# Optimization experiments

Hardware: AMD Instinct MI355X
Metric: run time of the kernel (lower is better)

Reference implementation:

```python
import jax, jax.numpy as jnp
import numpy as np

B, T, C, HS = 8, 2048, 1024, 128

def setup_inputs() -> dict:
    key = jax.random.key(0)
    kx, kq, kk, kv = jax.random.split(key, 4)
    x = jax.random.normal(kx, (B, T, C), dtype=jnp.float32)
    # torch Linear(C, HS, bias=False): y = x @ W^T with W [HS, C].
    # We store the transposed form [C, HS] and right-multiply (same math).
    scale = 1.0 / np.sqrt(C)  # torch default init scale-ish; exact init irrelevant for correctness
    Wq = jax.random.normal(kq, (C, HS), dtype=jnp.float32) * scale
    Wk = jax.random.normal(kk, (C, HS), dtype=jnp.float32) * scale
    Wv = jax.random.normal(kv, (C, HS), dtype=jnp.float32) * scale
    return {"x": x, "Wq": Wq, "Wk": Wk, "Wv": Wv}

def reference(x, Wq, Wk, Wv):
    Bx, Tx, Cx = x.shape
    q = x @ Wq  # [B, T, HS]
    k = x @ Wk
    v = x @ Wv
    # NOTE: original scales by C**-0.5 where C = n_embd (not head_size)
    wei = jnp.einsum('btd,bsd->bts', q, k) * (Cx ** -0.5)  # [B, T, T]
    causal = jnp.tril(jnp.ones((Tx, Tx), dtype=bool))
    wei = jnp.where(causal, wei, -jnp.inf)
    wei = jax.nn.softmax(wei, axis=-1)
    # dropout rate 0.0 (eval semantics) -> identity
    return jnp.einsum('bts,bsd->btd', wei, v)  # [B, T, HS]
```

## Files before the change

### kernel.cpp

```cpp
#include <hip/hip_runtime.h>
#include <hip/hip_bf16.h>
#include <stdint.h>

typedef float f32x4 __attribute__((ext_vector_type(4)));
typedef float f32x4v __attribute__((ext_vector_type(4)));
typedef short short8 __attribute__((ext_vector_type(8)));
typedef unsigned short u16;
typedef unsigned short u16x8 __attribute__((ext_vector_type(8)));
typedef unsigned short u16x4 __attribute__((ext_vector_type(4)));

#define MFMA16x16x32 __builtin_amdgcn_mfma_f32_16x16x32_bf16

__device__ __forceinline__ u16 f2bf(float f) {
    unsigned int u = __builtin_bit_cast(unsigned int, f);
    u += 0x7fffu + ((u >> 16) & 1u);
    return (u16)(u >> 16);
}
__device__ __forceinline__ float bf2f(u16 v) {
    unsigned int u = ((unsigned int)v) << 16;
    return __builtin_bit_cast(float, u);
}

__device__ __forceinline__ void gload_lds16(const void* g, void* l) {
    __builtin_amdgcn_global_load_lds(
        (const __attribute__((address_space(1))) uint32_t*)g,
        (__attribute__((address_space(3))) uint32_t*)l, 16, 0, 0);
}

__device__ __forceinline__ int z_small128(int p) {
    int na = (p + 2) >> 1;
    int za = (8 * na + 16) / 17;
    za = za < 1 ? 1 : za;
    return za > 7 ? 7 : za;
}

__global__ void k_transpose_wf(const float* __restrict__ Wq, const float* __restrict__ Wk,
                               const float* __restrict__ Wv, u16* __restrict__ WTf) {
    int tid  = blockIdx.x * 256 + threadIdx.x;
    int f    = tid >> 6;
    int lane = tid & 63;
    int kt  = f / 48;
    int rem = f % 48;
    int ks  = rem / 24;
    int nc  = rem % 24;
    int col = nc * 16 + (lane & 15);
    int w   = col >> 7, n = col & 127;
    int k0  = kt * 64 + ks * 32 + (lane >> 4) * 8;
    const float* W = (w == 0) ? Wq : ((w == 1) ? Wk : Wv);
    u16x8 v;
#pragma unroll
    for (int j = 0; j < 8; ++j)
        v[j] = f2bf(W[(size_t)(k0 + j) * 128 + n]);
    *(u16x8*)(&WTf[(size_t)tid * 8]) = v;
}

__global__ __launch_bounds__(512) void k_qkv_gemm8(
    const float* __restrict__ x, const u16* __restrict__ WTf,
    u16* __restrict__ qb, u16* __restrict__ kb, u16* __restrict__ vT)
{
    __shared__ u16 abuf[2][64 * 64];
    __shared__ u16 bbuf[2][384 * 64];
    const int tid  = threadIdx.x;
    const int lane = tid & 63, wid = tid >> 6;
    const int wr = wid >> 2, wc = wid & 3;
    const int lrow = lane & 15, lk = lane >> 4;
    const int m0 = blockIdx.x * 64;

    const int arow = tid >> 3;
    const int aseg = tid & 7;
    const float* xsrc = x + (size_t)(m0 + arow) * 1024 + aseg * 8;

    f32x4 acc[2][6];
#pragma unroll
    for (int i = 0; i < 2; ++i)
#pragma unroll
        for (int j = 0; j < 6; ++j) acc[i][j] = (f32x4){0.f, 0.f, 0.f, 0.f};

#define LOADA(s0, s1, ktv)                                                     \
    s0 = *(const f32x4v*)(xsrc + (ktv) * 64);                                  \
    s1 = *(const f32x4v*)(xsrc + (ktv) * 64 + 4);

#define STOREA(buf, s0, s1)                                                    \
    {   u16x8 v;                                                               \
        v[0]=f2bf(s0[0]); v[1]=f2bf(s0[1]); v[2]=f2bf(s0[2]); v[3]=f2bf(s0[3]); \
        v[4]=f2bf(s1[0]); v[5]=f2bf(s1[1]); v[6]=f2bf(s1[2]); v[7]=f2bf(s1[3]); \
        *(u16x8*)(&buf[arow * 64 + ((aseg ^ (arow & 7)) << 3)]) = v; }

#define ISSUEB(buf, ktv)                                                       \
    {   const u16* bsrc = WTf + (size_t)(ktv) * 24576;                         \
        _Pragma("unroll") for (int i = 0; i < 6; ++i) {                        \
            int c = tid + i * 512;                                             \
            gload_lds16(bsrc + c * 8, &buf[c * 8]);                            \
        } }

#define COMPUTE(ab, bb)                                                        \
    _Pragma("unroll") for (int ks = 0; ks < 2; ++ks) {                         \
        short8 af[2];                                                          \
        _Pragma("unroll") for (int mf = 0; mf < 2; ++mf) {                     \
            int row = wr * 32 + mf * 16 + lrow;                                \
            int blk = (ks * 4 + lk) ^ (row & 7);                               \
            af[mf] = *(const short8*)(&ab[row * 64 + (blk << 3)]);             \
        }                                                                      \
        _Pragma("unroll") for (int nf = 0; nf < 6; ++nf) {                     \
            short8 bfr = *(const short8*)(&bb[(ks * 24 + wc * 6 + nf) * 512 + lane * 8]); \
            _Pragma("unroll") for (int mf = 0; mf < 2; ++mf)                   \
                acc[mf][nf] = MFMA16x16x32(af[mf], bfr, acc[mf][nf], 0, 0, 0); \
        } }

#define WAITBAR()                                                              \
    asm volatile("s_waitcnt vmcnt(2) lgkmcnt(0)\n\ts_barrier" ::: "memory");   \
    __builtin_amdgcn_sched_barrier(0);

    f32x4v a0A, a1A, a0B, a1B;
    LOADA(a0A, a1A, 0);
    LOADA(a0B, a1B, 1);
    STOREA(abuf[0], a0A, a1A);
    ISSUEB(bbuf[0], 0);
    LOADA(a0A, a1A, 2);
    WAITBAR();

    for (int kt = 0; kt < 16; kt += 2) {
        {
            const int ktn = (kt + 1 < 16) ? kt + 1 : 15;
            ISSUEB(bbuf[1], ktn);
            __builtin_amdgcn_sched_barrier(0);
            COMPUTE(abuf[0], bbuf[0]);
            STOREA(abuf[1], a0B, a1B);
            const int kp = (kt + 3 < 16) ? kt + 3 : 15;
            LOADA(a0B, a1B, kp);
            WAITBAR();
        }
        {
            const int ktn = (kt + 2 < 16) ? kt + 2 : 15;
            ISSUEB(bbuf[0], ktn);
            __builtin_amdgcn_sched_barrier(0);
            COMPUTE(abuf[1], bbuf[1]);
            STOREA(abuf[0], a0A, a1A);
            const int kp = (kt + 4 < 16) ? kt + 4 : 15;
            LOADA(a0A, a1A, kp);
            WAITBAR();
        }
    }
#undef LOADA
#undef STOREA
#undef ISSUEB
#undef COMPUTE
#undef WAITBAR

#pragma unroll
    for (int nf = 0; nf < 6; ++nf) {
        const int gc   = wc * 96 + nf * 16 + lrow;
        const int wsel = gc >> 7;
        const int col  = gc & 127;
#pragma unroll
        for (int mf = 0; mf < 2; ++mf) {
            const int row0 = m0 + wr * 32 + mf * 16 + lk * 4;
            if (wsel == 0) {
#pragma unroll
                for (int jj = 0; jj < 4; ++jj)
                    qb[(size_t)(row0 + jj) * 128 + col] = f2bf(acc[mf][nf][jj]);
            } else if (wsel == 1) {
#pragma unroll
                for (int jj = 0; jj < 4; ++jj)
                    kb[(size_t)(row0 + jj) * 128 + col] = f2bf(acc[mf][nf][jj]);
            } else {
                const int bb = row0 >> 11, t0 = row0 & 2047;
                u16x4 v;
#pragma unroll
                for (int jj = 0; jj < 4; ++jj) v[jj] = f2bf(acc[mf][nf][jj]);
                *(u16x4*)(&vT[((size_t)bb * 128 + col) * 2048 + t0]) = v;
            }
        }
    }
}

__global__ __launch_bounds__(256) void k_flash9(
    const u16* __restrict__ qb, const u16* __restrict__ kb, const u16* __restrict__ vT,
    u16* __restrict__ po, float* __restrict__ pm, float* __restrict__ pl)
{
    __shared__ u16 k_lds[128 * 128];
    __shared__ u16 v_lds[128 * 128];
    __shared__ u16 p_lds[4 * 16 * 128];
    const int tid  = threadIdx.x;
    const int lane = tid & 63, wid = tid >> 6;
    const int lrow = lane & 15, lk = lane >> 4;
    const int bx = blockIdx.x;
    const int b  = bx & 7;
    const int p  = (bx >> 3) & 15;
    const int z  = bx >> 7;

    const int za = z_small128(p);
    int qt, n, k, Z;
    if (z < za) { qt = p;      n = (p + 2) >> 1;  k = z;      Z = za;     }
    else        { qt = 31 - p; n = (33 - p) >> 1; k = z - za; Z = 8 - za; }
    const int t0 = (k * n) / Z;
    const int t1 = ((k + 1) * n) / Z;

    const int qrow0 = qt * 64;
    short8 qf[4];
    {
        const u16* qp = qb + ((size_t)b * 2048 + qrow0 + wid * 16 + lrow) * 128;
#pragma unroll
        for (int ks = 0; ks < 4; ++ks) qf[ks] = *(const short8*)(qp + ks * 32 + lk * 8);
    }
    f32x4 of[8];
#pragma unroll
    for (int i = 0; i < 8; ++i) of[i] = (f32x4){0.f, 0.f, 0.f, 0.f};
    float mrun[4], lsum[4];
#pragma unroll
    for (int j = 0; j < 4; ++j) { mrun[j] = -1e30f; lsum[j] = 0.f; }

    const u16* kbase = kb + (size_t)b * 2048 * 128;
    const u16* vbase = vT + (size_t)b * 128 * 2048;
    u16* pw = p_lds + wid * (16 * 128);

    for (int t = t0; t < t1; ++t) {
        const int kv0 = t << 7;
        __syncthreads();
#pragma unroll
        for (int i = 0; i < 8; ++i) {
            int ch = tid + i * 256;
            int row = ch >> 4, blk = ch & 15;
            gload_lds16(kbase + (size_t)(kv0 + row) * 128 + ((blk ^ (row & 7)) << 3),
                        &k_lds[ch * 8]);
        }
#pragma unroll
        for (int i = 0; i < 8; ++i) {
            int ch = tid + i * 256;
            int row = ch >> 4, blk = ch & 15;
            gload_lds16(vbase + (size_t)row * 2048 + kv0 + ((blk ^ (row & 7)) << 3),
                        &v_lds[ch * 8]);
        }
        __syncthreads();

        f32x4 sf[8];
#pragma unroll
        for (int nf = 0; nf < 8; ++nf) sf[nf] = (f32x4){0.f, 0.f, 0.f, 0.f};
#pragma unroll
        for (int ks = 0; ks < 4; ++ks)
#pragma unroll
            for (int nf = 0; nf < 8; ++nf) {
                int row = nf * 16 + lrow;
                int blk = (ks * 4 + lk) ^ (row & 7);
                short8 bfr = *(const short8*)(&k_lds[row * 128 + (blk << 3)]);
                sf[nf] = MFMA16x16x32(qf[ks], bfr, sf[nf], 0, 0, 0);
            }

        const bool needmask = (kv0 + 127 > qrow0 + wid * 16);
#pragma unroll
        for (int nf = 0; nf < 8; ++nf)
#pragma unroll
            for (int jj = 0; jj < 4; ++jj) {
                float s = sf[nf][jj] * 0.03125f;
                if (needmask &&
                    (kv0 + nf * 16 + lrow > qrow0 + wid * 16 + lk * 4 + jj)) s = -1e30f;
                sf[nf][jj] = s;
            }
        float mt[4];
#pragma unroll
        for (int jj = 0; jj < 4; ++jj) {
            float m01 = fmaxf(sf[0][jj], sf[1][jj]);
            float m23 = fmaxf(sf[2][jj], sf[3][jj]);
            float m45 = fmaxf(sf[4][jj], sf[5][jj]);
            float m67 = fmaxf(sf[6][jj], sf[7][jj]);
            mt[jj] = fmaxf(fmaxf(m01, m23), fmaxf(m45, m67));
        }
#pragma unroll
        for (int off = 1; off < 16; off <<= 1)
#pragma unroll
            for (int jj = 0; jj < 4; ++jj)
                mt[jj] = fmaxf(mt[jj], __shfl_xor(mt[jj], off));
        bool small = true;
#pragma unroll
        for (int jj = 0; jj < 4; ++jj) small = small && (mt[jj] <= mrun[jj] + 8.f);
        if (!__all(small)) {
#pragma unroll
            for (int jj = 0; jj < 4; ++jj) {
                float mnew = fmaxf(mrun[jj], mt[jj]);
                float sc   = __expf(mrun[jj] - mnew);
                mrun[jj]   = mnew;
                lsum[jj]  *= sc;
#pragma unroll
                for (int df = 0; df < 8; ++df) of[df][jj] *= sc;
            }
        }
        float rs[4] = {0.f, 0.f, 0.f, 0.f};
#pragma unroll
        for (int nf = 0; nf < 8; ++nf)
#pragma unroll
            for (int jj = 0; jj < 4; ++jj) {
                float e = __expf(sf[nf][jj] - mrun[jj]);
                sf[nf][jj] = e;
                rs[jj] += e;
            }
#pragma unroll
        for (int off = 1; off < 16; off <<= 1)
#pragma unroll
            for (int jj = 0; jj < 4; ++jj)
                rs[jj] += __shfl_xor(rs[jj], off);
#pragma unroll
        for (int jj = 0; jj < 4; ++jj) lsum[jj] += rs[jj];

#pragma unroll
        for (int nf = 0; nf < 8; ++nf)
#pragma unroll
            for (int jj = 0; jj < 4; ++jj) {
                int row = lk * 4 + jj;
                int col = nf * 16 + lrow;
                pw[row * 128 + (((col >> 3) ^ (row & 7)) << 3) + (col & 7)] = f2bf(sf[nf][jj]);
            }
        asm volatile("s_waitcnt lgkmcnt(0)" ::: "memory");
        __builtin_amdgcn_sched_barrier(0);
        short8 paf[4];
#pragma unroll
        for (int ks2 = 0; ks2 < 4; ++ks2) {
            int blk = (ks2 * 4 + lk) ^ (lrow & 7);
            paf[ks2] = *(const short8*)(&pw[lrow * 128 + (blk << 3)]);
        }
#pragma unroll
        for (int ks2 = 0; ks2 < 4; ++ks2)
#pragma unroll
            for (int df = 0; df < 8; ++df) {
                int row = df * 16 + lrow;
                int blk = (ks2 * 4 + lk) ^ (row & 7);
                short8 vf = *(const short8*)(&v_lds[row * 128 + (blk << 3)]);
                of[df] = MFMA16x16x32(paf[ks2], vf, of[df], 0, 0, 0);
            }
    }

    u16* poslab = po + (size_t)bx * (64 * 128);
#pragma unroll
    for (int df = 0; df < 8; ++df)
#pragma unroll
        for (int jj = 0; jj < 4; ++jj)
            poslab[(size_t)(wid * 16 + lk * 4 + jj) * 128 + df * 16 + lrow] = f2bf(of[df][jj]);
    if (lrow == 0) {
#pragma unroll
        for (int jj = 0; jj < 4; ++jj) {
            pm[(size_t)bx * 64 + wid * 16 + lk * 4 + jj] = mrun[jj];
            pl[(size_t)bx * 64 + wid * 16 + lk * 4 + jj] = lsum[jj];
        }
    }
}

__global__ __launch_bounds__(256) void k_combine(
    const u16* __restrict__ po, const float* __restrict__ pm, const float* __restrict__ pl,
    float* __restrict__ out)
{
    const int row  = blockIdx.x * 4 + (threadIdx.x >> 6);
    const int lane = threadIdx.x & 63;
    const int b  = row >> 11;
    const int t  = row & 2047;
    const int qt = t >> 6;
    const int r  = t & 63;

    const int p  = (qt < 16) ? qt : 31 - qt;
    const int za = z_small128(p);
    const int zlo = (qt < 16) ? 0 : za;
    const int zhi = (qt < 16) ? za : 8;

    float M = -1e30f;
    for (int z = zlo; z < zhi; ++z)
        M = fmaxf(M, pm[(size_t)(b + 8 * p + 128 * z) * 64 + r]);
    float den = 0.f, a0 = 0.f, a1 = 0.f;
    for (int z = zlo; z < zhi; ++z) {
        const int bxp = b + 8 * p + 128 * z;
        const float w = __expf(pm[(size_t)bxp * 64 + r] - M);
        den += w * pl[(size_t)bxp * 64 + r];
        const u16* slab = po + ((size_t)bxp * 64 + r) * 128;
        a0 += w * bf2f(slab[lane]);
        a1 += w * bf2f(slab[lane + 64]);
    }
    const float inv = 1.f / den;
    out[(size_t)row * 128 + lane]      = a0 * inv;
    out[(size_t)row * 128 + lane + 64] = a1 * inv;
}

extern "C" void kernel_launch(void* const* d_in, const int* in_sizes, int n_in,
                              void* d_out, int out_size, void* d_ws, size_t ws_size,
                              hipStream_t stream) {
    const float* x  = (const float*)d_in[0];
    const float* Wq = (const float*)d_in[1];
    const float* Wk = (const float*)d_in[2];
    const float* Wv = (const float*)d_in[3];
    float* out = (float*)d_out;

    char* ws = (char*)d_ws;
    u16*   qb  = (u16*)(ws);
    u16*   kb  = (u16*)(ws + (size_t)4  * 1048576);
    u16*   vT  = (u16*)(ws + (size_t)8  * 1048576);
    u16*   WTf = (u16*)(ws + (size_t)12 * 1048576);
    u16*   po  = (u16*)(ws + (size_t)13 * 1048576);
    float* pm  = (float*)(ws + (size_t)47 * 1048576);
    float* pl  = (float*)(ws + (size_t)48 * 1048576);

    k_transpose_wf<<<192, 256, 0, stream>>>(Wq, Wk, Wv, WTf);
    k_qkv_gemm8<<<256, 512, 0, stream>>>(x, WTf, qb, kb, vT);
    k_flash9<<<1024, 256, 0, stream>>>(qb, kb, vT, po, pm, pl);
    k_combine<<<4096, 256, 0, stream>>>(po, pm, pl, out);
}
```

Measured before the change: 74.68 us.

## Retile QKV GEMM to 128-row by 192-column blocks split across N halves

```diff
diff --git a/kernel.cpp b/kernel.cpp
--- a/kernel.cpp
+++ b/kernel.cpp
@@ -54,21 +54,22 @@
     *(u16x8*)(&WTf[(size_t)tid * 8]) = v;
 }
 
-__global__ __launch_bounds__(512) void k_qkv_gemm8(
+__global__ __launch_bounds__(512) void k_qkv_gemm12(
     const float* __restrict__ x, const u16* __restrict__ WTf,
     u16* __restrict__ qb, u16* __restrict__ kb, u16* __restrict__ vT)
 {
-    __shared__ u16 abuf[2][64 * 64];
-    __shared__ u16 bbuf[2][384 * 64];
+    __shared__ u16 abuf[2][128 * 64];
+    __shared__ u16 bbuf[2][2 * 12 * 512];
     const int tid  = threadIdx.x;
     const int lane = tid & 63, wid = tid >> 6;
-    const int wr = wid >> 2, wc = wid & 3;
+    const int wr = wid >> 1, wc = wid & 1;
     const int lrow = lane & 15, lk = lane >> 4;
-    const int m0 = blockIdx.x * 64;
-
-    const int arow = tid >> 3;
-    const int aseg = tid & 7;
-    const float* xsrc = x + (size_t)(m0 + arow) * 1024 + aseg * 8;
+    const int nh = blockIdx.x & 1;
+    const int m0 = (blockIdx.x >> 1) * 128;
+
+    const int arow = tid >> 2;
+    const int aseg = tid & 3;
+    const float* xsrc = x + (size_t)(m0 + arow) * 1024 + aseg * 16;
 
     f32x4 acc[2][6];
 #pragma unroll
@@ -76,21 +77,29 @@
 #pragma unroll
         for (int j = 0; j < 6; ++j) acc[i][j] = (f32x4){0.f, 0.f, 0.f, 0.f};
 
-#define LOADA(s0, s1, ktv)                                                     \
-    s0 = *(const f32x4v*)(xsrc + (ktv) * 64);                                  \
-    s1 = *(const f32x4v*)(xsrc + (ktv) * 64 + 4);
-
-#define STOREA(buf, s0, s1)                                                    \
-    {   u16x8 v;                                                               \
-        v[0]=f2bf(s0[0]); v[1]=f2bf(s0[1]); v[2]=f2bf(s0[2]); v[3]=f2bf(s0[3]); \
-        v[4]=f2bf(s1[0]); v[5]=f2bf(s1[1]); v[6]=f2bf(s1[2]); v[7]=f2bf(s1[3]); \
-        *(u16x8*)(&buf[arow * 64 + ((aseg ^ (arow & 7)) << 3)]) = v; }
+#define LOADA(p0, p1, p2, p3, ktv)                                             \
+    p0 = *(const f32x4v*)(xsrc + (ktv) * 64);                                  \
+    p1 = *(const f32x4v*)(xsrc + (ktv) * 64 + 4);                              \
+    p2 = *(const f32x4v*)(xsrc + (ktv) * 64 + 8);                              \
+    p3 = *(const f32x4v*)(xsrc + (ktv) * 64 + 12);
+
+#define STOREA(buf, p0, p1, p2, p3)                                            \
+    {   u16x8 v0, v1;                                                          \
+        v0[0]=f2bf(p0[0]); v0[1]=f2bf(p0[1]); v0[2]=f2bf(p0[2]); v0[3]=f2bf(p0[3]); \
+        v0[4]=f2bf(p1[0]); v0[5]=f2bf(p1[1]); v0[6]=f2bf(p1[2]); v0[7]=f2bf(p1[3]); \
+        v1[0]=f2bf(p2[0]); v1[1]=f2bf(p2[1]); v1[2]=f2bf(p2[2]); v1[3]=f2bf(p2[3]); \
+        v1[4]=f2bf(p3[0]); v1[5]=f2bf(p3[1]); v1[6]=f2bf(p3[2]); v1[7]=f2bf(p3[3]); \
+        *(u16x8*)(&buf[arow * 64 + (((2*aseg)   ^ (arow & 7)) << 3)]) = v0;     \
+        *(u16x8*)(&buf[arow * 64 + (((2*aseg+1) ^ (arow & 7)) << 3)]) = v1; }
 
 #define ISSUEB(buf, ktv)                                                       \
-    {   const u16* bsrc = WTf + (size_t)(ktv) * 24576;                         \
-        _Pragma("unroll") for (int i = 0; i < 6; ++i) {                        \
-            int c = tid + i * 512;                                             \
-            gload_lds16(bsrc + c * 8, &buf[c * 8]);                            \
+    {   _Pragma("unroll") for (int i = 0; i < 3; ++i) {                        \
+            int c   = tid + i * 512;                              \
+            int ks_ = c / 768;                                                 \
+            int r_  = c - ks_ * 768;                               \
+            const u16* src = WTf + ((size_t)((ktv) * 2 + ks_) * 24 + nh * 12   \
+                                    + (r_ >> 6)) * 512 + (r_ & 63) * 8;        \
+            gload_lds16(src, &buf[c * 8]);                                     \
         } }
 
 #define COMPUTE(ab, bb)                                                        \
@@ -102,21 +111,21 @@
             af[mf] = *(const short8*)(&ab[row * 64 + (blk << 3)]);             \
         }                                                                      \
         _Pragma("unroll") for (int nf = 0; nf < 6; ++nf) {                     \
-            short8 bfr = *(const short8*)(&bb[(ks * 24 + wc * 6 + nf) * 512 + lane * 8]); \
+            short8 bfr = *(const short8*)(&bb[(ks * 12 + wc * 6 + nf) * 512 + lane * 8]); \
             _Pragma("unroll") for (int mf = 0; mf < 2; ++mf)                   \
                 acc[mf][nf] = MFMA16x16x32(af[mf], bfr, acc[mf][nf], 0, 0, 0); \
         } }
 
 #define WAITBAR()                                                              \
-    asm volatile("s_waitcnt vmcnt(2) lgkmcnt(0)\n\ts_barrier" ::: "memory");   \
+    asm volatile("s_waitcnt vmcnt(4) lgkmcnt(0)\n\ts_barrier" ::: "memory");   \
     __builtin_amdgcn_sched_barrier(0);
 
-    f32x4v a0A, a1A, a0B, a1B;
-    LOADA(a0A, a1A, 0);
-    LOADA(a0B, a1B, 1);
-    STOREA(abuf[0], a0A, a1A);
+    f32x4v a0A, a1A, a2A, a3A, a0B, a1B, a2B, a3B;
+    LOADA(a0A, a1A, a2A, a3A, 0);
+    LOADA(a0B, a1B, a2B, a3B, 1);
+    STOREA(abuf[0], a0A, a1A, a2A, a3A);
     ISSUEB(bbuf[0], 0);
-    LOADA(a0A, a1A, 2);
+    LOADA(a0A, a1A, a2A, a3A, 2);
     WAITBAR();
 
     for (int kt = 0; kt < 16; kt += 2) {
@@ -125,9 +134,9 @@
             ISSUEB(bbuf[1], ktn);
             __builtin_amdgcn_sched_barrier(0);
             COMPUTE(abuf[0], bbuf[0]);
-            STOREA(abuf[1], a0B, a1B);
+            STOREA(abuf[1], a0B, a1B, a2B, a3B);
             const int kp = (kt + 3 < 16) ? kt + 3 : 15;
-            LOADA(a0B, a1B, kp);
+            LOADA(a0B, a1B, a2B, a3B, kp);
             WAITBAR();
         }
         {
@@ -135,9 +144,9 @@
             ISSUEB(bbuf[0], ktn);
             __builtin_amdgcn_sched_barrier(0);
             COMPUTE(abuf[1], bbuf[1]);
-            STOREA(abuf[0], a0A, a1A);
+            STOREA(abuf[0], a0A, a1A, a2A, a3A);
             const int kp = (kt + 4 < 16) ? kt + 4 : 15;
-            LOADA(a0A, a1A, kp);
+            LOADA(a0A, a1A, a2A, a3A, kp);
             WAITBAR();
         }
     }
@@ -149,7 +158,7 @@
 
 #pragma unroll
     for (int nf = 0; nf < 6; ++nf) {
-        const int gc   = wc * 96 + nf * 16 + lrow;
+        const int gc   = nh * 192 + wc * 96 + nf * 16 + lrow;
         const int wsel = gc >> 7;
         const int col  = gc & 127;
 #pragma unroll
@@ -164,11 +173,11 @@
                 for (int jj = 0; jj < 4; ++jj)
                     kb[(size_t)(row0 + jj) * 128 + col] = f2bf(acc[mf][nf][jj]);
             } else {
-                const int bb = row0 >> 11, t0 = row0 & 2047;
+                const int bb2 = row0 >> 11, t0 = row0 & 2047;
                 u16x4 v;
 #pragma unroll
                 for (int jj = 0; jj < 4; ++jj) v[jj] = f2bf(acc[mf][nf][jj]);
-                *(u16x4*)(&vT[((size_t)bb * 128 + col) * 2048 + t0]) = v;
+                *(u16x4*)(&vT[((size_t)bb2 * 128 + col) * 2048 + t0]) = v;
             }
         }
     }
@@ -395,7 +404,7 @@
     float* pl  = (float*)(ws + (size_t)48 * 1048576);
 
     k_transpose_wf<<<192, 256, 0, stream>>>(Wq, Wk, Wv, WTf);
-    k_qkv_gemm8<<<256, 512, 0, stream>>>(x, WTf, qb, kb, vT);
+    k_qkv_gemm12<<<256, 512, 0, stream>>>(x, WTf, qb, kb, vT);
     k_flash9<<<1024, 256, 0, stream>>>(qb, kb, vT, po, pm, pl);
     k_combine<<<4096, 256, 0, stream>>>(po, pm, pl, out);
 }
```

Result: slower. 80.47 us (+7.8%).
